# Performance work log

Measured on AMD Instinct MI355X. Metric: run time of the kernel, lower is better.

The kernel has to match this reference:

```python
import jax, jax.numpy as jnp
import numpy as np

B, M, L = 8, 512, 1024          # batch, block_size, attn_lim (max span)
H, K = 512, 8                   # hidden, heads
D = H // K                      # head_dim = 64
RAMP = 32                       # attn_span_len (soft-mask ramp)
SPAN_INIT = 1.0                 # attn_span_init -> full span, skip_len = 0
SCALE = 1.0 / np.sqrt(D)


def _unskew(X):
    # X: [b, M, M+L] -> [b, M, L]  (relative-position unshift via reshape trick)
    b, m, ml = X.shape
    l = ml - m
    X = X.reshape(b, m * ml)
    X = jnp.pad(X, ((0, 0), (0, m)))
    X = X.reshape(b, m, ml + 1)
    return X[:, :, :l]


def _skew(X):
    # X: [b, M, L] -> [b, M, L+M]  (pad value 0)
    b, m, l = X.shape
    X = jnp.pad(X, ((0, 0), (0, 0), (0, m + 1)))
    X = X.reshape(b, -1)[:, : m * (l + m)]
    return X.reshape(b, m, l + m)


def _heads(x):
    # [B, S, H] -> [B*K, S, D]
    b, s, _ = x.shape
    return x.reshape(b, s, K, D).transpose(0, 2, 1, 3).reshape(b * K, s, D)


def setup_inputs() -> dict:
    key0 = jax.random.key(0)
    ks = jax.random.split(key0, 8)
    s = 0.02
    return {
        "query": jax.random.normal(ks[0], (B, M, H), jnp.float32),
        "key": jax.random.normal(ks[1], (B, M + L, H), jnp.float32),
        "value": jax.random.normal(ks[2], (B, M + L, H), jnp.float32),
        "key_pe": jax.random.normal(ks[3], (1, D, L), jnp.float32) * s,
        "Wq": jax.random.normal(ks[4], (H, H), jnp.float32) * s,
        "Wk": jax.random.normal(ks[5], (H, H), jnp.float32) * s,
        "Wv": jax.random.normal(ks[6], (H, H), jnp.float32) * s,
        "Wo": jax.random.normal(ks[7], (H, H), jnp.float32) * s,
        "span_val": jnp.full((K, 1, 1), SPAN_INIT, jnp.float32),
    }


def reference(query, key, value, key_pe, Wq, Wk, Wv, Wo, span_val):
    # QKV projections (nn.Linear, no bias: y = x @ W.T) + head split
    q = _heads(query @ Wq.T)     # [B*K, M, D]
    k = _heads(key @ Wk.T)       # [B*K, M+L, D]
    v = _heads(value @ Wv.T)     # [B*K, M+L, D]

    # content attention + unskew to relative coordinates
    attn_cont = _unskew(jnp.einsum('bmd,bnd->bmn', q, k))    # [B*K, M, L]
    # positional attention (shared across batch/heads via key_pe[1,D,L])
    attn_pos = jnp.einsum('bmd,dl->bml', q, key_pe[0])       # [B*K, M, L]

    attn = jax.nn.softmax((attn_cont + attn_pos) * SCALE, axis=-1)

    # adaptive span soft mask, per head (skip_len = 0)
    template = jnp.linspace(1.0 - L, 0.0, L, dtype=jnp.float32)        # [L]
    mask = jnp.clip((template + span_val * L) / RAMP + 1.0, 0.0, 1.0)  # [K,1,L]
    attn = (attn.reshape(B, K, M, L) * mask[None]).reshape(B * K, M, L)

    # skew back to absolute coords and contract with values
    out = jnp.matmul(_skew(attn), v)                         # [B*K, M, D]
    out = out.reshape(B, K, M, D).transpose(0, 2, 1, 3).reshape(B, M, H)
    return out @ Wo.T
```

## Files before the change

### kernel.cpp

```cpp
#include <hip/hip_runtime.h>
#include <hip/hip_bf16.h>
#include <type_traits>

typedef __hip_bfloat16 bf16;
typedef short bf16x8 __attribute__((ext_vector_type(8)));
typedef float f32x4 __attribute__((ext_vector_type(4)));
typedef short short4_ __attribute__((ext_vector_type(4)));

#define NB 8
#define SM 512
#define SL 1024
#define SH 512
#define NH 8
#define HD 64
#define SN 1536

static __device__ __forceinline__ short bf_bits(float x) {
  union { bf16 b; short s; } u; u.b = __float2bfloat16(x); return u.s;
}
static __device__ __forceinline__ bf16x8 ld8any(const bf16* p) {
  return *reinterpret_cast<const bf16x8*>(p);
}
static __device__ __forceinline__ bf16x8 ld8any(const float* p) {
  float4 a = *reinterpret_cast<const float4*>(p);
  float4 b = *reinterpret_cast<const float4*>(p + 4);
  bf16x8 r;
  r[0] = bf_bits(a.x); r[1] = bf_bits(a.y); r[2] = bf_bits(a.z); r[3] = bf_bits(a.w);
  r[4] = bf_bits(b.x); r[5] = bf_bits(b.y); r[6] = bf_bits(b.z); r[7] = bf_bits(b.w);
  return r;
}
static __device__ __forceinline__ void st1(bf16* p, float v) { *p = __float2bfloat16(v); }
static __device__ __forceinline__ void st1(float* p, float v) { *p = v; }
static __device__ __forceinline__ f32x4 mfma16(bf16x8 a, bf16x8 b, f32x4 c) {
  return __builtin_amdgcn_mfma_f32_16x16x32_bf16(a, b, c, 0, 0, 0);
}


__global__ __launch_bounds__(256) void prep_all(
    const float* __restrict__ key, const float* __restrict__ value,
    const float* __restrict__ query,
    const float* __restrict__ Wq, const float* __restrict__ Wk,
    const float* __restrict__ Wv, const float* __restrict__ Wo,
    const float* __restrict__ pe,
    bf16* __restrict__ kS, bf16* __restrict__ vS, bf16* __restrict__ qS,
    bf16* __restrict__ Wb, bf16* __restrict__ peF) {
  __shared__ __align__(16) bf16 t[16 * 520];
  const int id = blockIdx.x, tid = threadIdx.x;
  if (id < 1920) {
    const float* src; bf16* dst;
    if (id < 768)       { src = key   + (size_t)id * 8192;
                          dst = kS    + (size_t)id * 8192; }
    else if (id < 1536) { src = value + (size_t)(id - 768) * 8192;
                          dst = vS    + (size_t)(id - 768) * 8192; }
    else if (id < 1792) { src = query + (size_t)(id - 1536) * 8192;
                          dst = qS    + (size_t)(id - 1536) * 8192; }
    else {
      const int s = id - 1792;
      const float* ws_[4] = {Wq, Wk, Wv, Wo};
      src = ws_[s >> 5] + (size_t)(s & 31) * 8192;
      dst = Wb + (size_t)(s >> 5) * 262144 + (size_t)(s & 31) * 8192;
    }
#pragma unroll
    for (int j = 0; j < 4; ++j) {
      const int i = j * 2048 + tid * 8;
      const bf16x8 v = ld8any(src + i);
      *reinterpret_cast<bf16x8*>(&t[(i >> 9) * 520 + (i & 511)]) = v;
    }
    __syncthreads();
#pragma unroll
    for (int j = 0; j < 4; ++j) {
      const int a = j * 2048 + tid * 8;
      const int kt5 = a >> 9, rest = a & 511;
      const int q = rest >> 7, rowl = (rest >> 3) & 15;
      *reinterpret_cast<bf16x8*>(dst + a) =
          *reinterpret_cast<const bf16x8*>(&t[rowl * 520 + kt5 * 32 + q * 8]);
    }
  } else {
    const int idx = (id - 1920) * 256 + tid;
    const int l = idx >> 6, d = idx & 63;
    peF[(size_t)((l >> 4) * 2 + (d >> 5)) * 512
        + (size_t)((((d >> 3) & 3) * 16 + (l & 15)) * 8 + (d & 7))]
      = __float2bfloat16(pe[d * SL + l]);
  }
}

#define T2STR 136

#define GL2(AF, BF, KT)                                                      \
  {                                                                          \
    AF[0] = ld8any(xr +         (size_t)(KT) * 512);                         \
    AF[1] = ld8any(xr + 8192  + (size_t)(KT) * 512);                         \
    AF[2] = ld8any(xr + 16384 + (size_t)(KT) * 512);                         \
    AF[3] = ld8any(xr + 24576 + (size_t)(KT) * 512);                         \
    BF[0] = ld8any(wr +         (size_t)(KT) * 512);                         \
    BF[1] = ld8any(wr + 8192  + (size_t)(KT) * 512);                         \
    BF[2] = ld8any(wr + 16384 + (size_t)(KT) * 512);                         \
    BF[3] = ld8any(wr + 24576 + (size_t)(KT) * 512);                         \
  }

template <int MODE, typename TY>
static __device__ __forceinline__ void gemm_dev2(const bf16* __restrict__ XF,
                                                 const bf16* __restrict__ WF,
                                                 TY* __restrict__ Y,
                                                 int id, bf16* tile) {
  const int yblk = id & 3, xblk = id >> 2;
  const int tid  = threadIdx.x;
  const int lane = tid & 63, w = tid >> 6;
  const int col16 = lane & 15, quad = lane >> 4;
  const int lane8 = lane * 8;
  const int wm = w >> 1, wn = w & 1;
  const int m0 = xblk * 128 + wm * 64;
  const int n0 = yblk * 128 + wn * 64;
  const bf16* xr = XF + (size_t)(m0 >> 4) * 8192 + lane8;
  const bf16* wr = WF + (size_t)(n0 >> 4) * 8192 + lane8;
  f32x4 acc[4][4];
#pragma unroll
  for (int i = 0; i < 4; ++i)
#pragma unroll
    for (int j = 0; j < 4; ++j) acc[i][j] = f32x4{0.f,0.f,0.f,0.f};

  bf16x8 afA[4], bfA[4], afB[4], bfB[4];
  GL2(afA, bfA, 0);
  __builtin_amdgcn_sched_barrier(0);
#pragma unroll
  for (int kt = 0; kt < 16; kt += 2) {
    GL2(afB, bfB, kt + 1);
    __builtin_amdgcn_sched_barrier(0);
#pragma unroll
    for (int mt = 0; mt < 4; ++mt)
#pragma unroll
      for (int nt = 0; nt < 4; ++nt)
        acc[mt][nt] = mfma16(afA[mt], bfA[nt], acc[mt][nt]);
    const int ktn = (kt + 2 < 16) ? kt + 2 : kt;
    GL2(afA, bfA, ktn);
    __builtin_amdgcn_sched_barrier(0);
#pragma unroll
    for (int mt = 0; mt < 4; ++mt)
#pragma unroll
      for (int nt = 0; nt < 4; ++nt)
        acc[mt][nt] = mfma16(afB[mt], bfB[nt], acc[mt][nt]);
  }

  if constexpr (MODE == 0) {
#pragma unroll
    for (int mt = 0; mt < 4; ++mt)
#pragma unroll
      for (int r = 0; r < 4; ++r) {
        const int row = m0 + mt*16 + quad*4 + r;
        TY* yr = Y + (size_t)row * SH + n0 + col16;
#pragma unroll
        for (int nt = 0; nt < 4; ++nt) st1(yr + nt*16, acc[mt][nt][r]);
      }
  } else if constexpr (MODE == 1) {
    const int dq = col16 >> 3, de = col16 & 7;
    const int head = n0 >> 6;
#pragma unroll
    for (int mt = 0; mt < 4; ++mt)
#pragma unroll
      for (int r = 0; r < 4; ++r) {
        const int row = m0 + mt*16 + quad*4 + r;
        const int b = row / SN, sr = row - b * SN;
        bf16* yr = (bf16*)Y
            + (((size_t)(b*NH + head)*96 + (sr>>4))*2)*512
            + (size_t)((sr&15)*8 + de);
#pragma unroll
        for (int nt = 0; nt < 4; ++nt)
          yr[(nt>>1)*512 + ((nt&1)*2 + dq)*128] = __float2bfloat16(acc[mt][nt][r]);
      }
  } else if constexpr (MODE == 3) {
    const int dq = col16 >> 3, de = col16 & 7;
    const int c5b = n0 >> 5;
#pragma unroll
    for (int mt = 0; mt < 4; ++mt)
#pragma unroll
      for (int r = 0; r < 4; ++r) {
        bf16* yr = (bf16*)Y + (size_t)((m0>>4) + mt) * 8192
                 + (size_t)((quad*4 + r)*8 + de);
#pragma unroll
        for (int nt = 0; nt < 4; ++nt)
          yr[(c5b + (nt>>1))*512 + ((nt&1)*2 + dq)*128] = __float2bfloat16(acc[mt][nt][r]);
      }
  } else {
#pragma unroll
    for (int mt = 0; mt < 4; ++mt)
#pragma unroll
      for (int r = 0; r < 4; ++r) {
        const int row_loc = wm*64 + mt*16 + quad*4 + r;
#pragma unroll
        for (int nt = 0; nt < 4; ++nt) {
          const int d = wn*64 + nt*16 + col16;
          tile[d * T2STR + row_loc] = __float2bfloat16(acc[mt][nt][r]);
        }
      }
    __syncthreads();
    const int d  = tid >> 1;
    const int hq = tid & 1;
    const bf16* src = tile + d * T2STR + hq * 64;
    const int row0 = xblk*128 + hq*64;
    const int b = row0 / SN, sr0 = row0 - b * SN;
    const int head = yblk*2 + (d >> 6);
    const int dd = d & 63;
    bf16* dstF = (bf16*)Y + (((size_t)(b*NH + head)*4 + (dd>>4))*96)*256
               + (size_t)(dd&15)*8;
#pragma unroll
    for (int i = 0; i < 8; ++i) {
      const int key = sr0 + i*8;
      const size_t off = (size_t)(key>>4)*256 + (size_t)((key>>3)&1)*128;
      *reinterpret_cast<uint4*>(dstF + off) = reinterpret_cast<const uint4*>(src)[i];
    }
  }
}

__global__ __launch_bounds__(256, 2) void gemmKQ(
    const bf16* __restrict__ XK, const bf16* __restrict__ WK, bf16* __restrict__ YK,
    const bf16* __restrict__ XQ, const bf16* __restrict__ WQ, bf16* __restrict__ YQ) {
  __shared__ bf16 dummy[8];
  const int id = blockIdx.x;
  if (id < 384) gemm_dev2<1, bf16>(XK, WK, YK, id, dummy);
  else          gemm_dev2<3, bf16>(XQ, WQ, YQ, id - 384, dummy);
}

__global__ __launch_bounds__(256, 2) void gemmV(
    const bf16* __restrict__ XF, const bf16* __restrict__ WF, bf16* __restrict__ Y) {
  __shared__ __align__(16) bf16 tile[128 * T2STR];
  gemm_dev2<2, bf16>(XF, WF, Y, blockIdx.x, tile);
}

__global__ __launch_bounds__(256, 2) void gemmO(
    const bf16* __restrict__ XF, const bf16* __restrict__ WF, float* __restrict__ Y) {
  __shared__ bf16 dummy[8];
  gemm_dev2<0, float>(XF, WF, Y, blockIdx.x, dummy);
}

#define PSTR1 69
#define BSTR1 104

__global__ __launch_bounds__(64, 2) void attn1w(
    const bf16* __restrict__ qp, const bf16* __restrict__ Kh,
    const bf16* __restrict__ VT, const bf16* __restrict__ peT,
    const float* __restrict__ spanv, bf16* __restrict__ ctx) {
  __shared__ __align__(16) float pos_s[16 * PSTR1];
  __shared__ __align__(16) bf16  P_s[16 * BSTR1];

  const int id = blockIdx.x;
  const int h  = id & 7;
  const int s_ = id >> 3;
  const int m0 = (s_ & 31) * 16;
  const int b  = s_ >> 5;
  const int hb = b * 8 + h;
  const int lane  = threadIdx.x;
  const int col16 = lane & 15, quad = lane >> 4, kq = quad << 3;
  const int q4 = quad << 2;
  const int lane8 = lane * 8;

  for (int i = lane; i < 16 * BSTR1; i += 64)
    P_s[i] = __float2bfloat16(0.0f);

  const bf16* qb = qp + (size_t)((b*SM + m0) >> 4) * 8192 + h*1024 + lane8;
  const bf16x8 qf0 = ld8any(qb), qf1 = ld8any(qb + 512);

  const bf16* kbF = Kh + (size_t)hb * 98304 + lane8;
  const bf16* vbF = VT + (size_t)hb * 98304 + lane8;
  const bf16* pbF = peT + lane8;

  float Mrun = -1.0e30f, Srun = 0.0f;
  const float span1024 = spanv[h] * 1024.0f;
  f32x4 o[4];
#pragma unroll
  for (int dt = 0; dt < 4; ++dt) o[dt] = f32x4{0.f,0.f,0.f,0.f};

  bf16x8 kf[5][2], pf[4][2], vf[4][3];

  {
    const int tk0 = m0 >> 4;
#pragma unroll
    for (int t = 0; t < 5; ++t) {
      const bf16* kr = kbF + (size_t)(tk0 + t) * 1024;
      kf[t][0] = ld8any(kr); kf[t][1] = ld8any(kr + 512);
    }
#pragma unroll
    for (int t = 0; t < 4; ++t) {
      const bf16* pr = pbF + (size_t)t * 1024;
      pf[t][0] = ld8any(pr); pf[t][1] = ld8any(pr + 512);
    }
#pragma unroll
    for (int dt = 0; dt < 4; ++dt) {
      const bf16* v0 = vbF + (size_t)dt * 24576 + (size_t)tk0 * 256;
#pragma unroll
      for (int ks = 0; ks < 3; ++ks) vf[dt][ks] = ld8any(v0 + ks*512);
    }
    __builtin_amdgcn_sched_barrier(0);
  }

  const int posw = col16 * PSTR1 + q4;
  const int posr = col16 * (PSTR1 - 1) + q4;
  const int pww  = col16 * BSTR1 + q4;
  const int pwr  = col16 * BSTR1 + kq;

  for (int ch = 0; ch < 16; ++ch) {
    const int l0 = ch << 6;

    f32x4 pacc[4];
#pragma unroll
    for (int t = 0; t < 4; ++t) {
      f32x4 a = {0.f,0.f,0.f,0.f};
      a = mfma16(pf[t][0], qf0, a);
      a = mfma16(pf[t][1], qf1, a);
      pacc[t] = a;
    }
#pragma unroll
    for (int t = 0; t < 4; ++t)
#pragma unroll
      for (int r = 0; r < 4; ++r)
        pos_s[posw + 16*t + r] = pacc[t][r];

    f32x4 cacc[5];
#pragma unroll
    for (int t = 0; t < 5; ++t) {
      f32x4 a = {0.f,0.f,0.f,0.f};
      a = mfma16(kf[t][0], qf0, a);
      a = mfma16(kf[t][1], qf1, a);
      cacc[t] = a;
    }

    {
      const int l0n = (ch < 15) ? l0 + 64 : l0;
      const int tkn = (m0 + l0n) >> 4;
      const int tpn = l0n >> 4;
#pragma unroll
      for (int t = 0; t < 5; ++t) {
        const bf16* kr = kbF + (size_t)(tkn + t) * 1024;
        kf[t][0] = ld8any(kr); kf[t][1] = ld8any(kr + 512);
      }
#pragma unroll
      for (int t = 0; t < 4; ++t) {
        const bf16* pr = pbF + (size_t)(tpn + t) * 1024;
        pf[t][0] = ld8any(pr); pf[t][1] = ld8any(pr + 512);
      }
      __builtin_amdgcn_sched_barrier(0);
    }

    float sc[5][4];
    float mc = -1.0e30f;
#pragma unroll
    for (int t = 0; t < 5; ++t) {
      const f32x4 pv4 = *reinterpret_cast<const f32x4*>(&pos_s[posr + 16*t]);
#pragma unroll
      for (int r = 0; r < 4; ++r) {
        const int l = 16*t + q4 + r - col16;
        float v = (cacc[t][r] + pv4[r]) * 0.125f;
        v = ((unsigned)l < 64u) ? v : -1.0e30f;
        sc[t][r] = v;
        mc = fmaxf(mc, v);
      }
    }
    mc = fmaxf(mc, __shfl_xor(mc, 16));
    mc = fmaxf(mc, __shfl_xor(mc, 32));
    const float Mnew = fmaxf(Mrun, mc);
    const float alpha = __expf(Mrun - Mnew);
    float ls = 0.0f;
#pragma unroll
    for (int t = 0; t < 5; ++t) {
      short4_ pk;
#pragma unroll
      for (int r = 0; r < 4; ++r) {
        const float p = __expf(sc[t][r] - Mnew);
        ls += p;
        const float lg = (float)(l0 + 16*t + q4 + r - col16);
        float mv = (lg - 1023.0f + span1024) * 0.03125f + 1.0f;
        mv = fminf(fmaxf(mv, 0.0f), 1.0f);
        pk[r] = bf_bits(p * mv);
      }
      *reinterpret_cast<short4_*>(&P_s[pww + 16*t]) = pk;
    }
    ls += __shfl_xor(ls, 16);
    ls += __shfl_xor(ls, 32);
    Srun = Srun * alpha + ls;
    Mrun = Mnew;

#pragma unroll
    for (int dt = 0; dt < 4; ++dt)
#pragma unroll
      for (int r = 0; r < 4; ++r) o[dt][r] *= alpha;
#pragma unroll
    for (int ks = 0; ks < 3; ++ks) {
      const bf16x8 ap = ld8any(&P_s[pwr + ks*32]);
#pragma unroll
      for (int dt = 0; dt < 4; ++dt)
        o[dt] = mfma16(vf[dt][ks], ap, o[dt]);
    }

    {
      const int tkn = (m0 + ((ch < 15) ? l0 + 64 : l0)) >> 4;
#pragma unroll
      for (int dt = 0; dt < 4; ++dt) {
        const bf16* v0 = vbF + (size_t)dt * 24576 + (size_t)tkn * 256;
#pragma unroll
        for (int ks = 0; ks < 3; ++ks) vf[dt][ks] = ld8any(v0 + ks*512);
      }
      __builtin_amdgcn_sched_barrier(0);
    }
  }

  const float inv = 1.0f / Srun;
  bf16* crb = ctx + (size_t)((b*SM + m0) >> 4) * 8192
            + (size_t)(h*1024 + (quad>>1)*128 + col16*8 + (quad&1)*4);
#pragma unroll
  for (int dt = 0; dt < 4; ++dt) {
    short4_ pk;
#pragma unroll
    for (int r = 0; r < 4; ++r) pk[r] = bf_bits(o[dt][r] * inv);
    *reinterpret_cast<short4_*>(crb + (size_t)(dt>>1)*512 + (dt&1)*256) = pk;
  }
}

template <int MODE, typename TX, typename TW, typename TY>
__global__ __launch_bounds__(256) void gemmbn64(const TX* __restrict__ X,
                                                const TW* __restrict__ W,
                                                TY* __restrict__ Y) {
  __shared__ __align__(16) bf16 tile[(MODE == 2) ? 64 * T2STR : 8];
  const int id   = blockIdx.x;
  const int s_   = id >> 3;
  const int xblk = (id & 7) + 8 * (s_ >> 3);
  const int yblk = s_ & 7;
  const int tid  = threadIdx.x;
  const int lane = tid & 63, w = tid >> 6;
  const int col16 = lane & 15, quad = lane >> 4, kq = quad << 3;
  const int wm = w >> 1, wn = w & 1;
  const int m0 = xblk * 128 + wm * 64;
  const int n0 = yblk * 64 + wn * 32;
  const TX* xr = X + (size_t)(m0 + col16) * SH + kq;
  const TW* wr = W + (size_t)(n0 + col16) * SH + kq;
  f32x4 acc[4][2];
#pragma unroll
  for (int i = 0; i < 4; ++i)
#pragma unroll
    for (int j = 0; j < 2; ++j) acc[i][j] = f32x4{0.f,0.f,0.f,0.f};
#pragma unroll
  for (int k0 = 0; k0 < SH; k0 += 32) {
    bf16x8 af[4], bfr[2];
#pragma unroll
    for (int t = 0; t < 4; ++t) af[t]  = ld8any(xr + (size_t)(t*16) * SH + k0);
#pragma unroll
    for (int t = 0; t < 2; ++t) bfr[t] = ld8any(wr + (size_t)(t*16) * SH + k0);
#pragma unroll
    for (int mt = 0; mt < 4; ++mt)
#pragma unroll
      for (int nt = 0; nt < 2; ++nt)
        acc[mt][nt] = mfma16(af[mt], bfr[nt], acc[mt][nt]);
  }

  if constexpr (MODE == 0) {
#pragma unroll
    for (int mt = 0; mt < 4; ++mt)
#pragma unroll
      for (int r = 0; r < 4; ++r) {
        const int row = m0 + mt*16 + quad*4 + r;
        TY* yr = Y + (size_t)row * SH + n0 + col16;
        st1(yr,      acc[mt][0][r]);
        st1(yr + 16, acc[mt][1][r]);
      }
  } else if constexpr (MODE == 1) {
#pragma unroll
    for (int mt = 0; mt < 4; ++mt)
#pragma unroll
      for (int r = 0; r < 4; ++r) {
        const int row = m0 + mt*16 + quad*4 + r;
        const int b = row / SN, sr = row - b * SN;
        bf16* yr = (bf16*)Y + (size_t)((b*NH + yblk)*SN + sr) * HD
                 + wn*32 + col16;
        yr[0]  = __float2bfloat16(acc[mt][0][r]);
        yr[16] = __float2bfloat16(acc[mt][1][r]);
      }
  } else {
#pragma unroll
    for (int mt = 0; mt < 4; ++mt)
#pragma unroll
      for (int r = 0; r < 4; ++r) {
        const int row_loc = wm*64 + mt*16 + quad*4 + r;
#pragma unroll
        for (int nt = 0; nt < 2; ++nt) {
          const int d = wn*32 + nt*16 + col16;
          tile[d * T2STR + row_loc] = __float2bfloat16(acc[mt][nt][r]);
        }
      }
    __syncthreads();
    const int d  = tid >> 2;
    const int hq = tid & 3;
    const bf16* src = tile + d * T2STR + hq * 32;
    const int row0 = xblk*128 + hq*32;
    const int b = row0 / SN, sr0 = row0 - b * SN;
    bf16* dst = (bf16*)Y + (size_t)((b*NH + yblk)*HD + d) * SN + sr0;
#pragma unroll
    for (int i = 0; i < 4; ++i)
      reinterpret_cast<uint4*>(dst)[i] = reinterpret_cast<const uint4*>(src)[i];
  }
}

__global__ void transpose_pe_fb(const float* __restrict__ pe, bf16* __restrict__ peT) {
  int idx = blockIdx.x * 256 + threadIdx.x;
  int l = idx >> 6, d = idx & 63;
  peT[idx] = __float2bfloat16(pe[d * SL + l]);
}

#define MT 16
#define CSTR 84
#define PSTR 65
#define BSTR 104
#define QSTR 72

__global__ __launch_bounds__(128) void attn_kernel_fb(
    const float* __restrict__ query, const float* __restrict__ Wq,
    const bf16* __restrict__ Kh, const bf16* __restrict__ VT,
    const bf16* __restrict__ peT, const float* __restrict__ spanv,
    bf16* __restrict__ ctx) {
  __shared__ __align__(16) float cont_lds[MT][CSTR];
  __shared__ __align__(16) float pos_lds[MT][PSTR];
  __shared__ __align__(16) bf16  P_lds[MT][BSTR];
  __shared__ __align__(16) bf16  q_lds[MT*QSTR];
  __shared__ float alpha_lds[MT];
  __shared__ float S_lds[MT];

  const int id = blockIdx.x;
  const int h  = id & 7;
  const int s_ = id >> 3;
  const int m0 = (s_ & 31) * MT;
  const int b  = s_ >> 5;
  const int hb = b * 8 + h;
  const int tid  = threadIdx.x;
  const int lane = tid & 63;
  const int w    = tid >> 6;
  const int col16 = lane & 15, quad = lane >> 4, kq = quad << 3;
  const int wr = quad << 2;

  for (int i = tid; i < MT * BSTR; i += 128)
    (&P_lds[0][0])[i] = __float2bfloat16(0.0f);

  bf16x8 qf0, qf1;
  {
    f32x4 qa0 = {0.f,0.f,0.f,0.f}, qa1 = qa0;
    const float* xq = query + (size_t)(b*SM + m0 + col16) * SH + kq;
    const float* w0 = Wq + (size_t)(h*HD + w*32 + col16) * SH + kq;
    const float* w1 = w0 + (size_t)16 * SH;
#pragma unroll
    for (int k0 = 0; k0 < SH; k0 += 32) {
      bf16x8 xa = ld8any(xq + k0);
      qa0 = mfma16(xa, ld8any(w0 + k0), qa0);
      qa1 = mfma16(xa, ld8any(w1 + k0), qa1);
    }
#pragma unroll
    for (int r = 0; r < 4; ++r) {
      q_lds[(wr + r)*QSTR + w*32 + col16]      = __float2bfloat16(qa0[r]);
      q_lds[(wr + r)*QSTR + w*32 + 16 + col16] = __float2bfloat16(qa1[r]);
    }
    __syncthreads();
    qf0 = ld8any(&q_lds[col16*QSTR + kq]);
    qf1 = ld8any(&q_lds[col16*QSTR + kq + 32]);
  }

  const bf16* kb = Kh + (size_t)(hb * SN) * HD + kq;
  const bf16* vb = VT + (size_t)(hb * HD) * SN;

  const int srow = tid >> 3, sj = tid & 7;
  float Mrun = -1.0e30f, Srun = 0.0f;
  const float span = spanv[h];
  const int dt0 = w * 16, dt1 = (w + 2) * 16;
  f32x4 o0 = {0.f,0.f,0.f,0.f}, o1 = o0;

  for (int ch = 0; ch < 16; ++ch) {
    const int l0 = ch << 6;
    const int nb_ = m0 + l0;

    f32x4 ca0 = {0.f,0.f,0.f,0.f}, ca1 = ca0, ca2 = ca0, pa0 = ca0, pa1 = ca0;
    {
      const bf16* kr0 = kb + (size_t)(nb_ + w*16 + col16) * HD;
      ca0 = mfma16(qf0, ld8any(kr0),           ca0);
      ca0 = mfma16(qf1, ld8any(kr0 + 32),      ca0);
      const bf16* kr1 = kr0 + 32 * HD;
      ca1 = mfma16(qf0, ld8any(kr1),           ca1);
      ca1 = mfma16(qf1, ld8any(kr1 + 32),      ca1);
      if (w == 0) {
        const bf16* kr2 = kr0 + 64 * HD;
        ca2 = mfma16(qf0, ld8any(kr2),         ca2);
        ca2 = mfma16(qf1, ld8any(kr2 + 32),    ca2);
      }
      const bf16* pr0 = peT + (size_t)(l0 + w*16 + col16) * HD + kq;
      pa0 = mfma16(qf0, ld8any(pr0),           pa0);
      pa0 = mfma16(qf1, ld8any(pr0 + 32),      pa0);
      const bf16* pr1 = pr0 + 32 * HD;
      pa1 = mfma16(qf0, ld8any(pr1),           pa1);
      pa1 = mfma16(qf1, ld8any(pr1 + 32),      pa1);
    }
#pragma unroll
    for (int r = 0; r < 4; ++r) {
      cont_lds[wr + r][w*16 + col16]      = ca0[r];
      cont_lds[wr + r][w*16 + 32 + col16] = ca1[r];
      if (w == 0) cont_lds[wr + r][64 + col16] = ca2[r];
      pos_lds[wr + r][w*16 + col16]       = pa0[r];
      pos_lds[wr + r][w*16 + 32 + col16]  = pa1[r];
    }
    __syncthreads();

    float sc[8];
    float mc = -1.0e30f;
    const float* crow = &cont_lds[srow][srow + sj*8];
    const float* prow = &pos_lds[srow][sj*8];
#pragma unroll
    for (int i = 0; i < 8; ++i) {
      float v = (crow[i] + prow[i]) * 0.125f;
      sc[i] = v;
      mc = fmaxf(mc, v);
    }
    mc = fmaxf(mc, __shfl_xor(mc, 1));
    mc = fmaxf(mc, __shfl_xor(mc, 2));
    mc = fmaxf(mc, __shfl_xor(mc, 4));
    const float Mnew = fmaxf(Mrun, mc);
    const float alpha = __expf(Mrun - Mnew);
    float ls = 0.0f;
    bf16* pwrow = &P_lds[srow][srow + sj*8];
#pragma unroll
    for (int i = 0; i < 8; ++i) {
      float p = __expf(sc[i] - Mnew);
      ls += p;
      const float tpl = (float)(l0 + sj*8 + i) - 1023.0f;
      float mv = (tpl + span * 1024.0f) * 0.03125f + 1.0f;
      mv = fminf(fmaxf(mv, 0.0f), 1.0f);
      pwrow[i] = __float2bfloat16(p * mv);
    }
    ls += __shfl_xor(ls, 1);
    ls += __shfl_xor(ls, 2);
    ls += __shfl_xor(ls, 4);
    Srun = Srun * alpha + ls;
    Mrun = Mnew;
    if (sj == 0) { alpha_lds[srow] = alpha; S_lds[srow] = Srun; }
    __syncthreads();

    float al[4];
#pragma unroll
    for (int r = 0; r < 4; ++r) al[r] = alpha_lds[wr + r];
#pragma unroll
    for (int r = 0; r < 4; ++r) { o0[r] *= al[r]; o1[r] *= al[r]; }
#pragma unroll
    for (int ks = 0; ks < 3; ++ks) {
      const bf16x8 ap = ld8any(&P_lds[col16][ks*32 + kq]);
      const bf16* v0 = vb + (size_t)(dt0 + col16) * SN + nb_ + ks*32 + kq;
      const bf16* v1 = vb + (size_t)(dt1 + col16) * SN + nb_ + ks*32 + kq;
      o0 = mfma16(ap, ld8any(v0), o0);
      o1 = mfma16(ap, ld8any(v1), o1);
    }
  }

  bf16* cr = ctx + (size_t)(b*SM + m0 + wr) * SH + h*HD + col16;
#pragma unroll
  for (int r = 0; r < 4; ++r) {
    const float inv = 1.0f / S_lds[wr + r];
    cr[(size_t)r * SH + dt0] = __float2bfloat16(o0[r] * inv);
    cr[(size_t)r * SH + dt1] = __float2bfloat16(o1[r] * inv);
  }
}

extern "C" void kernel_launch(void* const* d_in, const int* in_sizes, int n_in,
                              void* d_out, int out_size, void* d_ws, size_t ws_size,
                              hipStream_t stream) {
  const float* query  = (const float*)d_in[0];
  const float* key    = (const float*)d_in[1];
  const float* value  = (const float*)d_in[2];
  const float* key_pe = (const float*)d_in[3];
  const float* Wq     = (const float*)d_in[4];
  const float* Wk     = (const float*)d_in[5];
  const float* Wv     = (const float*)d_in[6];
  const float* Wo     = (const float*)d_in[7];
  const float* spanv  = (const float*)d_in[8];
  float* out = (float*)d_out;

  bf16* ws = (bf16*)d_ws;
  if (ws_size >= (size_t)48365568) {
    bf16* B0   = ws;
    bf16* B1   = B0  + 6291456;
    bf16* B2   = B1  + 6291456;
    bf16* qp   = B2  + 6291456;
    bf16* ctxC = qp  + 2097152;
    bf16* peF  = ctxC + 2097152;
    bf16* Wb   = peF + 65536;
    bf16* Wq_b = Wb, *Wk_b = Wb + 262144, *Wv_b = Wb + 524288, *Wo_b = Wb + 786432;

    prep_all<<<1952, 256, 0, stream>>>(key, value, query, Wq, Wk, Wv, Wo,
                                       key_pe, B0, B1, ctxC, Wb, peF);
    gemmKQ<<<512, 256, 0, stream>>>(B0, Wk_b, B2, ctxC, Wq_b, qp);
    gemmV<<<384, 256, 0, stream>>>(B1, Wv_b, B0);
    attn1w<<<2048, 64, 0, stream>>>(qp, B2, B0, peF, spanv, ctxC);
    gemmO<<<128, 256, 0, stream>>>(ctxC, Wo_b, out);
  } else {
    bf16* k_head = ws;
    bf16* vT     = k_head + 6291456;
    bf16* ctx    = vT     + 6291456;
    bf16* peT    = ctx    + 2097152;
    gemmbn64<1, float, float, bf16><<<768, 256, 0, stream>>>(key,   Wk, k_head);
    gemmbn64<2, float, float, bf16><<<768, 256, 0, stream>>>(value, Wv, vT);
    transpose_pe_fb<<<256, 256, 0, stream>>>(key_pe, peT);
    attn_kernel_fb<<<2048, 128, 0, stream>>>(query, Wq, k_head, vT,
                                             peT, spanv, ctx);
    gemmbn64<0, bf16, float, float><<<256, 256, 0, stream>>>(ctx, Wo, out);
  }
}
```

Before: 186.2 us.

## Defer softmax rescaling, precompute mask biases, and retile output GEMM with register prefetch

The attention kernel now skips the running-max rescale of the output accumulator and sum whenever no lane's new max exceeds the old one by more than a threshold (lazy rescaling). It also precomputes per-lane causal biases and span-mask bases so the inner loop avoids index arithmetic. The output projection GEMM is replaced with a dedicated 128x64-tile kernel launched on twice as many blocks, double-buffering fragments in registers straight from global memory. Deferred rescaling lets exponentials grow up to e^8 before renormalising, which slightly raises overflow and precision risk in the bf16 probabilities.

After: 183.7 us. Within noise of the previous version (-1.3%).

```diff
diff --git a/kernel.cpp b/kernel.cpp
--- a/kernel.cpp
+++ b/kernel.cpp
@@ -226,10 +226,67 @@
   gemm_dev2<2, bf16>(XF, WF, Y, blockIdx.x, tile);
 }
 
+#define GLO(AF, BF, KT)                                                      \
+  {                                                                          \
+    AF[0] = ld8any(xr +         (size_t)(KT) * 512);                         \
+    AF[1] = ld8any(xr + 8192  + (size_t)(KT) * 512);                         \
+    AF[2] = ld8any(xr + 16384 + (size_t)(KT) * 512);                         \
+    AF[3] = ld8any(xr + 24576 + (size_t)(KT) * 512);                         \
+    BF[0] = ld8any(wr +         (size_t)(KT) * 512);                         \
+    BF[1] = ld8any(wr + 8192  + (size_t)(KT) * 512);                         \
+  }
+
 __global__ __launch_bounds__(256, 2) void gemmO(
     const bf16* __restrict__ XF, const bf16* __restrict__ WF, float* __restrict__ Y) {
-  __shared__ bf16 dummy[8];
-  gemm_dev2<0, float>(XF, WF, Y, blockIdx.x, dummy);
+  const int id   = blockIdx.x;
+  const int s_   = id >> 3;
+  const int xblk = (id & 7) + 8 * (s_ >> 3);
+  const int yblk = s_ & 7;
+  const int tid  = threadIdx.x;
+  const int lane = tid & 63, w = tid >> 6;
+  const int col16 = lane & 15, quad = lane >> 4;
+  const int lane8 = lane * 8;
+  const int wm = w >> 1, wn = w & 1;
+  const int m0 = xblk * 128 + wm * 64;
+  const int n0 = yblk * 64 + wn * 32;
+  const bf16* xr = XF + (size_t)(m0 >> 4) * 8192 + lane8;
+  const bf16* wr = WF + (size_t)(n0 >> 4) * 8192 + lane8;
+  f32x4 acc[4][2];
+#pragma unroll
+  for (int i = 0; i < 4; ++i)
+#pragma unroll
+    for (int j = 0; j < 2; ++j) acc[i][j] = f32x4{0.f,0.f,0.f,0.f};
+
+  bf16x8 afA[4], bfA[2], afB[4], bfB[2];
+  GLO(afA, bfA, 0);
+  __builtin_amdgcn_sched_barrier(0);
+#pragma unroll
+  for (int kt = 0; kt < 16; kt += 2) {
+    GLO(afB, bfB, kt + 1);
+    __builtin_amdgcn_sched_barrier(0);
+#pragma unroll
+    for (int mt = 0; mt < 4; ++mt)
+#pragma unroll
+      for (int nt = 0; nt < 2; ++nt)
+        acc[mt][nt] = mfma16(afA[mt], bfA[nt], acc[mt][nt]);
+    const int ktn = (kt + 2 < 16) ? kt + 2 : kt;
+    GLO(afA, bfA, ktn);
+    __builtin_amdgcn_sched_barrier(0);
+#pragma unroll
+    for (int mt = 0; mt < 4; ++mt)
+#pragma unroll
+      for (int nt = 0; nt < 2; ++nt)
+        acc[mt][nt] = mfma16(afB[mt], bfB[nt], acc[mt][nt]);
+  }
+#pragma unroll
+  for (int mt = 0; mt < 4; ++mt)
+#pragma unroll
+    for (int r = 0; r < 4; ++r) {
+      const int row = m0 + mt*16 + quad*4 + r;
+      float* yr = Y + (size_t)row * SH + n0 + col16;
+      yr[0]  = acc[mt][0][r];
+      yr[16] = acc[mt][1][r];
+    }
 }
 
 #define PSTR1 69
@@ -269,6 +326,19 @@
 #pragma unroll
   for (int dt = 0; dt < 4; ++dt) o[dt] = f32x4{0.f,0.f,0.f,0.f};
 
+  float bias_[5][4], mvs_[5][4];
+  {
+    const float mvb = ((float)(q4 - col16 - 1023) + span1024) * 0.03125f + 1.0f;
+#pragma unroll
+    for (int t = 0; t < 5; ++t)
+#pragma unroll
+      for (int r = 0; r < 4; ++r) {
+        const int l = 16*t + q4 + r - col16;
+        bias_[t][r] = ((unsigned)l < 64u) ? 0.0f : -1.0e30f;
+        mvs_[t][r]  = mvb + (float)(16*t + r) * 0.03125f;
+      }
+  }
+
   bf16x8 kf[5][2], pf[4][2], vf[4][3];
 
   {
@@ -347,9 +417,7 @@
       const f32x4 pv4 = *reinterpret_cast<const f32x4*>(&pos_s[posr + 16*t]);
 #pragma unroll
       for (int r = 0; r < 4; ++r) {
-        const int l = 16*t + q4 + r - col16;
-        float v = (cacc[t][r] + pv4[r]) * 0.125f;
-        v = ((unsigned)l < 64u) ? v : -1.0e30f;
+        const float v = fmaf(cacc[t][r] + pv4[r], 0.125f, bias_[t][r]);
         sc[t][r] = v;
         mc = fmaxf(mc, v);
       }
@@ -357,17 +425,18 @@
     mc = fmaxf(mc, __shfl_xor(mc, 16));
     mc = fmaxf(mc, __shfl_xor(mc, 32));
     const float Mnew = fmaxf(Mrun, mc);
-    const float alpha = __expf(Mrun - Mnew);
+    const bool defer = __all(Mnew - Mrun <= 8.0f);
+    const float Mb = defer ? Mrun : Mnew;
+    const float chf = (float)ch * 2.0f;
     float ls = 0.0f;
 #pragma unroll
     for (int t = 0; t < 5; ++t) {
       short4_ pk;
 #pragma unroll
       for (int r = 0; r < 4; ++r) {
-        const float p = __expf(sc[t][r] - Mnew);
+        const float p = __expf(sc[t][r] - Mb);
         ls += p;
-        const float lg = (float)(l0 + 16*t + q4 + r - col16);
-        float mv = (lg - 1023.0f + span1024) * 0.03125f + 1.0f;
+        float mv = mvs_[t][r] + chf;
         mv = fminf(fmaxf(mv, 0.0f), 1.0f);
         pk[r] = bf_bits(p * mv);
       }
@@ -375,13 +444,19 @@
     }
     ls += __shfl_xor(ls, 16);
     ls += __shfl_xor(ls, 32);
-    Srun = Srun * alpha + ls;
-    Mrun = Mnew;
-
-#pragma unroll
-    for (int dt = 0; dt < 4; ++dt)
-#pragma unroll
-      for (int r = 0; r < 4; ++r) o[dt][r] *= alpha;
+
+    if (defer) {
+      Srun += ls;
+    } else {
+      const float alpha = __expf(Mrun - Mnew);
+      Srun = Srun * alpha + ls;
+      Mrun = Mnew;
+#pragma unroll
+      for (int dt = 0; dt < 4; ++dt)
+#pragma unroll
+        for (int r = 0; r < 4; ++r) o[dt][r] *= alpha;
+    }
+
 #pragma unroll
     for (int ks = 0; ks < 3; ++ks) {
       const bf16x8 ap = ld8any(&P_s[pwr + ks*32]);
@@ -689,7 +764,7 @@
     gemmKQ<<<512, 256, 0, stream>>>(B0, Wk_b, B2, ctxC, Wq_b, qp);
     gemmV<<<384, 256, 0, stream>>>(B1, Wv_b, B0);
     attn1w<<<2048, 64, 0, stream>>>(qp, B2, B0, peF, spanv, ctxC);
-    gemmO<<<128, 256, 0, stream>>>(ctxC, Wo_b, out);
+    gemmO<<<256, 256, 0, stream>>>(ctxC, Wo_b, out);
   } else {
     bf16* k_head = ws;
     bf16* vT     = k_head + 6291456;
```
